# Kernel optimization log

Measured on AMD Instinct MI355X. Metric: run time of the kernel, lower is better.

The kernel has to match this reference:

```python
import jax, jax.numpy as jnp
import numpy as np

B, S, D, OUT, CLS = 131072, 14, 16, 128, 7
EPS = 1e-5
SCALING = 1.0


def _layer_norm(x, g, b):
    # torch LayerNorm over last dim, biased variance
    m = jnp.mean(x, axis=-1, keepdims=True)
    v = jnp.mean((x - m) ** 2, axis=-1, keepdims=True)
    return (x - m) * jax.lax.rsqrt(v + EPS) * g + b


def setup_inputs() -> dict:
    key = jax.random.key(0)
    ks = jax.random.split(key, 20)
    p = lambda k, shp: jax.random.normal(k, shp, dtype=jnp.float32) * 0.05
    inp = {
        "sample": jax.random.normal(ks[0], (B, S, D), dtype=jnp.float32),
        # affine LayerNorms on state(query)/stored(key)/pattern-projection(value) inputs
        "ln_q_g": jnp.ones((D,), jnp.float32), "ln_q_b": jnp.zeros((D,), jnp.float32),
        "ln_k_g": jnp.ones((D,), jnp.float32), "ln_k_b": jnp.zeros((D,), jnp.float32),
        "ln_v_g": jnp.ones((D,), jnp.float32), "ln_v_b": jnp.zeros((D,), jnp.float32),
        # Hopfield association core projections (num_heads=1, head_dim=16)
        "Wq": p(ks[1], (D, D)), "bq": p(ks[2], (D,)),
        "Wk": p(ks[3], (D, D)), "bk": p(ks[4], (D,)),
        "Wv": p(ks[5], (D, D)), "bv": p(ks[6], (D,)),
        # Hopfield output projection 16 -> 128
        "Wo": p(ks[7], (OUT, D)), "bo": p(ks[8], (OUT,)),
        # Linear_m: 14 -> 1
        "Wm": p(ks[9], (1, S)), "bm": p(ks[10], (1,)),
        # Linear_b: 128 -> 7
        "Wb": p(ks[11], (CLS, OUT)), "bb": p(ks[12], (CLS,)),
    }
    return inp


def reference(sample, ln_q_g, ln_q_b, ln_k_g, ln_k_b, ln_v_g, ln_v_b,
              Wq, bq, Wk, bk, Wv, bv, Wo, bo, Wm, bm, Wb, bb):
    # --- Hopfield self-association (single update step) ---
    q_in = _layer_norm(sample, ln_q_g, ln_q_b)   # state pattern
    k_in = _layer_norm(sample, ln_k_g, ln_k_b)   # stored pattern
    v_in = _layer_norm(sample, ln_v_g, ln_v_b)   # pattern projection
    Q = jnp.einsum('bsd,ed->bse', q_in, Wq) + bq  # (B,S,16)
    K = jnp.einsum('bsd,ed->bse', k_in, Wk) + bk
    V = jnp.einsum('bsd,ed->bse', v_in, Wv) + bv
    A = jax.nn.softmax(SCALING * jnp.einsum('bqd,bkd->bqk', Q, K), axis=-1)  # (B,S,S)
    O = jnp.einsum('bqk,bkd->bqd', A, V)          # (B,S,16)
    x = jnp.einsum('bsd,od->bso', O, Wo) + bo     # (B,S,128)
    # --- head: transpose, Linear_m over seq dim, transpose, Linear_b ---
    x = jnp.swapaxes(x, 1, 2)                     # (B,128,S)
    y = jnp.einsum('bos,ms->bom', x, Wm) + bm     # (B,128,1)
    y = jnp.swapaxes(y, 1, 2)                     # (B,1,128)
    z = jnp.einsum('bmo,co->bmc', y, Wb) + bb     # (B,1,7)
    return jax.nn.softmax(z, axis=-1)
```

## Files before the change

kernel.cpp:

```cpp
#include <hip/hip_runtime.h>


#define NBATCH 131072
#define NWAVES 8192
#define ITERF  ((size_t)NWAVES * 896)

typedef float    f32x4 __attribute__((ext_vector_type(4)));
typedef _Float16 f16x4 __attribute__((ext_vector_type(4)));
typedef __fp16   h16x2 __attribute__((ext_vector_type(2)));

#define ROR(x,N) __int_as_float(__builtin_amdgcn_update_dpp(0, __float_as_int(x), 0x120 + (N), 0xF, 0xF, false))

static __device__ __forceinline__ f16x4 cvt4(float a, float b, float c, float d) {
    union { f16x4 v; h16x2 h[2]; } u;
    u.h[0] = __builtin_amdgcn_cvt_pkrtz(a, b);
    u.h[1] = __builtin_amdgcn_cvt_pkrtz(c, d);
    return u.v;
}

static __device__ __forceinline__ f32x4 mfma16(f16x4 a, f16x4 b, f32x4 c) {
#if __has_builtin(__builtin_amdgcn_mfma_f32_16x16x16f16)
    return __builtin_amdgcn_mfma_f32_16x16x16f16(a, b, c, 0, 0, 0);
#else
    f32x4 d;
    asm("v_mfma_f32_16x16x16_f16 %0, %1, %2, %3" : "=v"(d) : "v"(a), "v"(b), "v"(c));
    return d;
#endif
}

__global__ __launch_bounds__(256) void hop_prep(
    const float* __restrict__ gq, const float* __restrict__ bq_ln,
    const float* __restrict__ gk,
    const float* __restrict__ gv, const float* __restrict__ bv_ln,
    const float* __restrict__ Wq, const float* __restrict__ bq,
    const float* __restrict__ Wk,
    const float* __restrict__ Wv, const float* __restrict__ bv,
    const float* __restrict__ Wo, const float* __restrict__ bo,
    const float* __restrict__ Wm, const float* __restrict__ bm,
    const float* __restrict__ Wb, const float* __restrict__ bb,
    float* __restrict__ ws)
{
    const float L2E = 1.4426950408889634f;
    __shared__ float WqP[256], WkP[256], WvP[256];
    __shared__ float bqP[16], bvP[16], WcS[112];
    const int t = threadIdx.x;
    {
        const int d = t & 15;
        WqP[t] = Wq[t] * gq[d];
        WkP[t] = Wk[t] * gk[d];
        WvP[t] = Wv[t] * gv[d];
    }
    if (t < 16) {
        float a = bq[t], c = bv[t];
        for (int d = 0; d < 16; ++d) {
            a = fmaf(Wq[t*16+d], bq_ln[d], a);
            c = fmaf(Wv[t*16+d], bv_ln[d], c);
        }
        bqP[t] = a; bvP[t] = c;
    }
    if (t < 112) {
        const int c = t >> 4, e = t & 15;
        float s = 0.f;
        for (int o = 0; o < 128; ++o) s = fmaf(Wb[c*128+o], Wo[o*16+e], s);
        WcS[t] = s;
    }
    __syncthreads();
    {
        const int dd = t >> 4, d = t & 15;
        float m = 0.f;
        for (int e = 0; e < 16; ++e) m = fmaf(WqP[e*16+d], WkP[e*16+dd], m);
        ws[t] = m * L2E;
    }
    if (t < 16) {
        float rr = 0.f;
        for (int e = 0; e < 16; ++e) rr = fmaf(bqP[e], WkP[e*16+t], rr);
        ws[256 + t] = rr * L2E;
    }
    {
        const int c = t >> 4, d = t & 15;
        float s = 0.f;
        if (c < 7)
            for (int e = 0; e < 16; ++e) s = fmaf(WcS[c*16+e], WvP[e*16+d], s);
        ws[272 + t] = s;
    }
    if (t < 16) {
        float v = 0.f;
        if (t < 7) {
            float wmsum = 0.f;
            for (int s = 0; s < 14; ++s) wmsum += Wm[s];
            float s1 = 0.f;
            for (int e = 0; e < 16; ++e) s1 = fmaf(WcS[t*16+e], bvP[e], s1);
            float s2 = 0.f, s3 = 0.f;
            for (int o = 0; o < 128; ++o) { s2 = fmaf(Wb[t*128+o], bo[o], s2); s3 += Wb[t*128+o]; }
            v = wmsum*s1 + wmsum*s2 + bm[0]*s3 + bb[t];
        }
        ws[528 + t] = v * L2E;
        ws[544 + t] = (t < 14) ? Wm[t] * L2E : 0.0f;
    }
}

__global__ __launch_bounds__(256, 4) void hop_main(const float* __restrict__ smp,
                                                   const float* __restrict__ W,
                                                   float* __restrict__ out)
{
    const int wave = (blockIdx.x * 256 + threadIdx.x) >> 6;
    const int l    = threadIdx.x & 63;
    const int col  = l & 15;
    const int q    = l >> 4;

    const float4 mt  = *reinterpret_cast<const float4*>(W + col*16 + q*4);
    const float4 w2  = *reinterpret_cast<const float4*>(W + 272 + col*16 + q*4);
    const float4 r4  = *reinterpret_cast<const float4*>(W + 256 + q*4);
    const float4 wm4 = *reinterpret_cast<const float4*>(W + 544 + q*4);
    const float  c2_l = W[528 + col];
    const f16x4 mtA  = cvt4(mt.x, mt.y, mt.z, mt.w);
    const f16x4 w2B  = cvt4(w2.x, w2.y, w2.z, w2.w);
    const f16x4 ONE  = {(_Float16)1.0f, (_Float16)1.0f, (_Float16)1.0f, (_Float16)1.0f};
    const f16x4 SIXT = {(_Float16)0.0625f, (_Float16)0.0625f, (_Float16)0.0625f, (_Float16)0.0625f};
    const f32x4 zero = {0.f, 0.f, 0.f, 0.f};
    const f32x4 rC   = {r4.x, r4.y, r4.z, r4.w};
    const f32x4 c2C  = {c2_l, c2_l, c2_l, c2_l};
    const bool  hi   = (q == 3);

    const int srow = (col < 14) ? col : 13;
    const float* p0 = smp + (size_t)wave * 896 + srow * 16 + q * 4;
    float* op = out + ((size_t)wave * 4 + q) * 7 + col;
    const size_t OSTEP = (size_t)NWAVES * 4 * 7;

    auto zbatch = [&](const f32x4& x) -> float {
        const f16x4 xf  = cvt4(x[0], x[1], x[2], x[3]);
        const f16x4 xqf = cvt4(x[0]*x[0], x[1]*x[1], x[2]*x[2], x[3]*x[3]);
        const f32x4 S1 = mfma16(SIXT, xf,  zero);
        const f32x4 S2 = mfma16(SIXT, xqf, zero);
        const float mean = S1[0];
        const float var  = fmaf(-mean, mean, S2[0]);
        const float rstd = __builtin_amdgcn_rsqf(var + 1e-5f);
        const float nmr  = -mean * rstd;
        const f16x4 xhA = cvt4(fmaf(x[0], rstd, nmr), fmaf(x[1], rstd, nmr),
                               fmaf(x[2], rstd, nmr), fmaf(x[3], rstd, nmr));
        const f32x4 P = mfma16(xhA, w2B, zero);
        const f32x4 T  = mfma16(mtA, xhA, rC);
        const f16x4 B2 = cvt4(T[0], T[1], T[2], T[3]);
        const f32x4 SS = mfma16(xhA, B2, zero);
        const float e0 = __builtin_amdgcn_exp2f(SS[0]);
        const float e1 = __builtin_amdgcn_exp2f(SS[1]);
        const float e2 = hi ? 0.0f : __builtin_amdgcn_exp2f(SS[2]);
        const float e3 = hi ? 0.0f : __builtin_amdgcn_exp2f(SS[3]);
        const f16x4 E  = cvt4(e0, e1, e2, e3);
        const f16x4 Pf = cvt4(P[0], P[1], P[2], P[3]);
        const f32x4 Zt = mfma16(E, ONE, zero);
        const f32x4 G  = mfma16(E, Pf,  zero);
        const float w0 = wm4.x * __builtin_amdgcn_rcpf(Zt[0]);
        const float w1 = wm4.y * __builtin_amdgcn_rcpf(Zt[1]);
        const float w2s = wm4.z * __builtin_amdgcn_rcpf(Zt[2]);
        const float w3 = wm4.w * __builtin_amdgcn_rcpf(Zt[3]);
        const f16x4 wA = cvt4(w0, w1, w2s, w3);
        const f16x4 Gf = cvt4(G[0], G[1], G[2], G[3]);
        const f32x4 ZZ = mfma16(wA, Gf, c2C);
        return ZZ[0];
    };

    auto epilogue = [&](float z0, float z1, float z2, float z3, float* o) {
        float z = (q == 1) ? z1 : z0;
        z = (q == 2) ? z2 : z;
        z = (q == 3) ? z3 : z;
        float e = (col < 7) ? __builtin_amdgcn_exp2f(z) : 0.0f;
        float s = e;
        s += ROR(s, 1); s += ROR(s, 2); s += ROR(s, 4); s += ROR(s, 8);
        if (col < 7) __builtin_nontemporal_store(e * __builtin_amdgcn_rcpf(s), o);
    };

#define LD4(v0, v1, v2, v3, it) { const float* pp = p0 + (size_t)(it) * ITERF; \
    v0 = __builtin_nontemporal_load(reinterpret_cast<const f32x4*>(pp));        \
    v1 = __builtin_nontemporal_load(reinterpret_cast<const f32x4*>(pp + 224));  \
    v2 = __builtin_nontemporal_load(reinterpret_cast<const f32x4*>(pp + 448));  \
    v3 = __builtin_nontemporal_load(reinterpret_cast<const f32x4*>(pp + 672)); }

    f32x4 a0, a1, a2, a3, b0, b1, b2, b3;
    LD4(a0, a1, a2, a3, 0);
    LD4(b0, b1, b2, b3, 1);
    epilogue(zbatch(a0), zbatch(a1), zbatch(a2), zbatch(a3), op);
    LD4(a0, a1, a2, a3, 2);
    epilogue(zbatch(b0), zbatch(b1), zbatch(b2), zbatch(b3), op + OSTEP);
    LD4(b0, b1, b2, b3, 3);
    epilogue(zbatch(a0), zbatch(a1), zbatch(a2), zbatch(a3), op + 2*OSTEP);
    epilogue(zbatch(b0), zbatch(b1), zbatch(b2), zbatch(b3), op + 3*OSTEP);
#undef LD4
}

extern "C" void kernel_launch(void* const* d_in, const int* in_sizes, int n_in,
                              void* d_out, int out_size, void* d_ws, size_t ws_size,
                              hipStream_t stream) {
    (void)in_sizes; (void)n_in; (void)out_size; (void)ws_size;
    const float* smp = (const float*)d_in[0];
    float* ws = (float*)d_ws;
    hop_prep<<<1, 256, 0, stream>>>(
        (const float*)d_in[1],  (const float*)d_in[2],
        (const float*)d_in[3],
        (const float*)d_in[5],  (const float*)d_in[6],
        (const float*)d_in[7],  (const float*)d_in[8],
        (const float*)d_in[9],
        (const float*)d_in[11], (const float*)d_in[12],
        (const float*)d_in[13], (const float*)d_in[14],
        (const float*)d_in[15], (const float*)d_in[16],
        (const float*)d_in[17], (const float*)d_in[18],
        ws);
    hop_main<<<NWAVES * 64 / 256, 256, 0, stream>>>(smp, ws, (float*)d_out);
}
```

Baseline: 31.73 us.

## Process one batch group per wave with 4x more waves and higher occupancy

Drops the per-wave loop over four iterations with software-pipelined double-buffered loads. Each wave now handles a single group of 4 batches, the grid grows fourfold, and launch bounds are raised to 8 blocks per CU to hide memory latency through occupancy. Scheduling barriers are placed between the per-batch computations. The trade is extra launch and wave-setup overhead (the weight loads are repeated per wave) and possible register pressure under the tighter bound, in exchange for more memory-level parallelism.

Result: no change. 31.58 us (-0.5%).

```diff
diff --git a/kernel.cpp b/kernel.cpp
--- a/kernel.cpp
+++ b/kernel.cpp
@@ -2,8 +2,6 @@
 
 
 #define NBATCH 131072
-#define NWAVES 8192
-#define ITERF  ((size_t)NWAVES * 896)
 
 typedef float    f32x4 __attribute__((ext_vector_type(4)));
 typedef _Float16 f16x4 __attribute__((ext_vector_type(4)));
@@ -99,7 +97,7 @@
     }
 }
 
-__global__ __launch_bounds__(256, 4) void hop_main(const float* __restrict__ smp,
+__global__ __launch_bounds__(256, 8) void hop_main(const float* __restrict__ smp,
                                                    const float* __restrict__ W,
                                                    float* __restrict__ out)
 {
@@ -125,7 +123,6 @@
     const int srow = (col < 14) ? col : 13;
     const float* p0 = smp + (size_t)wave * 896 + srow * 16 + q * 4;
     float* op = out + ((size_t)wave * 4 + q) * 7 + col;
-    const size_t OSTEP = (size_t)NWAVES * 4 * 7;
 
     auto zbatch = [&](const f32x4& x) -> float {
         const f16x4 xf  = cvt4(x[0], x[1], x[2], x[3]);
@@ -160,32 +157,26 @@
         return ZZ[0];
     };
 
-    auto epilogue = [&](float z0, float z1, float z2, float z3, float* o) {
-        float z = (q == 1) ? z1 : z0;
-        z = (q == 2) ? z2 : z;
-        z = (q == 3) ? z3 : z;
-        float e = (col < 7) ? __builtin_amdgcn_exp2f(z) : 0.0f;
-        float s = e;
-        s += ROR(s, 1); s += ROR(s, 2); s += ROR(s, 4); s += ROR(s, 8);
-        if (col < 7) __builtin_nontemporal_store(e * __builtin_amdgcn_rcpf(s), o);
-    };
-
-#define LD4(v0, v1, v2, v3, it) { const float* pp = p0 + (size_t)(it) * ITERF; \
-    v0 = __builtin_nontemporal_load(reinterpret_cast<const f32x4*>(pp));        \
-    v1 = __builtin_nontemporal_load(reinterpret_cast<const f32x4*>(pp + 224));  \
-    v2 = __builtin_nontemporal_load(reinterpret_cast<const f32x4*>(pp + 448));  \
-    v3 = __builtin_nontemporal_load(reinterpret_cast<const f32x4*>(pp + 672)); }
-
-    f32x4 a0, a1, a2, a3, b0, b1, b2, b3;
-    LD4(a0, a1, a2, a3, 0);
-    LD4(b0, b1, b2, b3, 1);
-    epilogue(zbatch(a0), zbatch(a1), zbatch(a2), zbatch(a3), op);
-    LD4(a0, a1, a2, a3, 2);
-    epilogue(zbatch(b0), zbatch(b1), zbatch(b2), zbatch(b3), op + OSTEP);
-    LD4(b0, b1, b2, b3, 3);
-    epilogue(zbatch(a0), zbatch(a1), zbatch(a2), zbatch(a3), op + 2*OSTEP);
-    epilogue(zbatch(b0), zbatch(b1), zbatch(b2), zbatch(b3), op + 3*OSTEP);
-#undef LD4
+    const f32x4 a0 = __builtin_nontemporal_load(reinterpret_cast<const f32x4*>(p0));
+    const f32x4 a1 = __builtin_nontemporal_load(reinterpret_cast<const f32x4*>(p0 + 224));
+    const f32x4 a2 = __builtin_nontemporal_load(reinterpret_cast<const f32x4*>(p0 + 448));
+    const f32x4 a3 = __builtin_nontemporal_load(reinterpret_cast<const f32x4*>(p0 + 672));
+
+    const float z0 = zbatch(a0);
+    __builtin_amdgcn_sched_barrier(0);
+    const float z1 = zbatch(a1);
+    __builtin_amdgcn_sched_barrier(0);
+    const float z2 = zbatch(a2);
+    __builtin_amdgcn_sched_barrier(0);
+    const float z3 = zbatch(a3);
+
+    float z = (q == 1) ? z1 : z0;
+    z = (q == 2) ? z2 : z;
+    z = (q == 3) ? z3 : z;
+    float e = (col < 7) ? __builtin_amdgcn_exp2f(z) : 0.0f;
+    float s = e;
+    s += ROR(s, 1); s += ROR(s, 2); s += ROR(s, 4); s += ROR(s, 8);
+    if (col < 7) __builtin_nontemporal_store(e * __builtin_amdgcn_rcpf(s), op);
 }
 
 extern "C" void kernel_launch(void* const* d_in, const int* in_sizes, int n_in,
@@ -205,5 +196,5 @@
         (const float*)d_in[15], (const float*)d_in[16],
         (const float*)d_in[17], (const float*)d_in[18],
         ws);
-    hop_main<<<NWAVES * 64 / 256, 256, 0, stream>>>(smp, ws, (float*)d_out);
-}
+    hop_main<<<NBATCH * 16 / 256, 256, 0, stream>>>(smp, ws, (float*)d_out);
+}
```
